# Kernel tuning notes

Measured on AMD Instinct MI355X. Metric: run time of the kernel, lower is better.

The kernel has to match this reference:

```python
import jax, jax.numpy as jnp
import numpy as np

N_NODES = 10000
N_EDGES = 160000
C = 64        # latent channels
H = 512       # MLP hidden width
L = 2         # allegro layers
NB = 8        # bessel basis size
CUT = 2.0     # radial cutoff
AVG = 3.0     # avg_num_neighbors


def setup_inputs() -> dict:
    key = jax.random.key(0)
    ks = jax.random.split(key, 12)
    positions = jax.random.normal(ks[0], (N_NODES, 3), jnp.float32)
    species = jax.random.randint(ks[1], (N_NODES,), 0, 2, jnp.int32)
    senders = jax.random.randint(ks[2], (N_EDGES,), 0, N_NODES, jnp.int32)
    receivers = jax.random.randint(ks[3], (N_EDGES,), 0, N_NODES, jnp.int32)
    w = lambda k, shape, fan: (jax.random.normal(k, shape, jnp.float32) / np.sqrt(fan).astype(np.float32))
    return dict(
        positions=positions,
        W_emb1=w(ks[4], (NB + 4, H), NB + 4),
        W_emb2=w(ks[5], (H, C), H),
        W_v=w(ks[6], (C, C), C),
        W_env=w(ks[7], (L, C, C), C),
        W_lat1=w(ks[8], (L, 3 * C, H), 3 * C),
        W_lat2=w(ks[9], (L, H, C), H),
        W_mix=w(ks[10], (L, C, 2 * C), C),
        W_out=w(ks[11], (C,), C),
        species=species, senders=senders, receivers=receivers,
    )


def reference(positions, W_emb1, W_emb2, W_v, W_env, W_lat1, W_lat2, W_mix, W_out,
              species, senders, receivers):
    node_attrs = jax.nn.one_hot(species, 2, dtype=positions.dtype)   # [N,2]
    r = positions[receivers] - positions[senders]                    # [E,3] edge vectors ('1o')
    d = jnp.sqrt(jnp.sum(r * r, axis=-1))                            # [E]
    dsafe = jnp.maximum(d, 1e-6)
    u = r / dsafe[:, None]                                           # unit vectors = l=1 spherical harmonics

    # radial basis: Bessel functions with smooth polynomial cutoff envelope
    xc = d / CUT
    env = jnp.where(xc < 1.0, (1.0 - xc ** 2) ** 2, 0.0)             # [E]
    nvec = jnp.arange(1, NB + 1, dtype=positions.dtype)
    bessel = jnp.sqrt(2.0 / CUT) * jnp.sin(nvec * jnp.pi * xc[:, None]) / dsafe[:, None]
    rad = bessel * env[:, None]                                      # [E,NB]

    # two-body latent embedding
    feat = jnp.concatenate([rad, node_attrs[senders], node_attrs[receivers]], axis=-1)  # [E,NB+4]
    x = (jax.nn.silu(feat @ W_emb1) @ W_emb2) * env[:, None]         # [E,C]
    # initial equivariant edge features (C channels of 1o)
    V = (x @ W_v)[:, :, None] * u[:, None, :]                        # [E,C,3]

    inv_sqrt2 = 1.0 / jnp.sqrt(2.0)
    for l in range(L):
        # environment density: scatter edge basis to sender nodes, gather back per edge
        w_e = x @ W_env[l]                                           # [E,C]
        rho1 = jax.ops.segment_sum(w_e[:, :, None] * u[:, None, :], senders,
                                   num_segments=N_NODES) / AVG       # [N,C,3] (1o density)
        rho0 = jax.ops.segment_sum(w_e, senders, num_segments=N_NODES) / AVG  # [N,C] (0e density)
        rho1_e = rho1[senders]                                       # [E,C,3]
        rho0_e = rho0[senders]                                       # [E,C]

        # channel-wise Clebsch-Gordan tensor products (lmax=1 paths)
        tp_scal = jnp.einsum('eci,eci->ec', V, rho1_e)               # 1o x 1o -> 0e
        tp_vec1 = V * rho0_e[:, :, None]                             # 1o x 0e -> 1o
        tp_vec2 = jnp.cross(V, rho1_e)                               # 1o x 1o -> 1e

        # latent update (residual, envelope-gated)
        lat_in = jnp.concatenate([x, tp_scal, rho0_e], axis=-1)      # [E,3C]
        dx = (jax.nn.silu(lat_in @ W_lat1[l]) @ W_lat2[l]) * env[:, None]
        x = (x + dx) * inv_sqrt2

        # equivariant update: latent-conditioned mix of tensor-product outputs
        mix = x @ W_mix[l]                                           # [E,2C]
        V = mix[:, :C, None] * tp_vec1 + mix[:, C:, None] * tp_vec2  # [E,C,3]

    # per-edge scalar readout, scatter-reduced to nodes
    e_edge = (x @ W_out) * env                                       # [E]
    node_energy = jax.ops.segment_sum(e_edge, receivers, num_segments=N_NODES) / AVG
    return node_energy
```

## Files before the change

### kernel.cpp

```cpp
#include <hip/hip_runtime.h>
#include <hip/hip_bf16.h>

#define E_NUM 160000
#define NN 10000
#define PI_F 3.14159265358979323846f

using u16 = unsigned short;
using u32 = unsigned int;
typedef short bf16x8 __attribute__((ext_vector_type(8)));
typedef float f32x4 __attribute__((ext_vector_type(4)));
typedef u32 u32x4 __attribute__((ext_vector_type(4)));

__device__ __forceinline__ float silu_fast(float z) {
    return z * __builtin_amdgcn_rcpf(1.0f + __expf(-z));
}
__device__ __forceinline__ float bfb2f(u32 bits16) {
    return __builtin_bit_cast(float, bits16 << 16);
}
__device__ __forceinline__ u32 f2bfb(float f) {
    return (u32)__builtin_bit_cast(u16, __float2bfloat16(f));
}
__device__ __forceinline__ u32 pack2(float lo, float hi) {
    return f2bfb(lo) | (f2bfb(hi) << 16);
}

__global__ void k_detect(const u16* __restrict__ posraw, int* __restrict__ flag) {
    int i = blockIdx.x * 256 + threadIdx.x;
    if (i >= 15000) return;
    float v = bfb2f((u32)posraw[2 * i]);
    if (!(fabsf(v) < 1e4f)) atomicOr(flag, 1);
}

__global__ void k_cvt_all(const void* s0, const void* s1, const void* s2,
                          const void* s3, const void* s4, const void* s5,
                          const void* s6, const void* s7, const void* s8,
                          float* __restrict__ dst, const int* __restrict__ flag) {
    int i = blockIdx.x * 256 + threadIdx.x;
    if (i >= 359792) return;
    const void* src; int off;
    if      (i < 30000)  { src = s0; off = i; }
    else if (i < 36144)  { src = s1; off = i - 30000; }
    else if (i < 68912)  { src = s2; off = i - 36144; }
    else if (i < 73008)  { src = s3; off = i - 68912; }
    else if (i < 81200)  { src = s4; off = i - 73008; }
    else if (i < 277808) { src = s5; off = i - 81200; }
    else if (i < 343344) { src = s6; off = i - 277808; }
    else if (i < 359728) { src = s7; off = i - 343344; }
    else                 { src = s8; off = i - 359728; }
    if (*flag) dst[i] = ((const float*)src)[off];
    else       dst[i] = bfb2f((u32)((const u16*)src)[off]);
}

__global__ void k_pack(const float* __restrict__ W, int K, int Nshift,
                       u16* __restrict__ pk) {
    int i = blockIdx.x * 256 + threadIdx.x;
    int total = K << Nshift;
    if (i >= total) return;
    int k = i >> Nshift, n = i & ((1 << Nshift) - 1);
    float w = W[i];
    u16 h = (u16)f2bfb(w);
    float r = w - bfb2f((u32)h);
    int idx = ((((k >> 3) << Nshift) + n) << 4) + (k & 7);
    pk[idx] = h; pk[idx + 8] = (u16)f2bfb(r);
}

__global__ void k_pack_emb1(const float* __restrict__ W , u16* __restrict__ pk) {
    int i = blockIdx.x * 256 + threadIdx.x;
    if (i >= 64 * 512) return;
    int k = i >> 9, n = i & 511;
    u16 out = 0;
    if (k < 24) {
        out = (u16)f2bfb(W[(k % 12) * 512 + n]);
    } else if (k < 36) {
        float w = W[(k - 24) * 512 + n];
        u16 h = (u16)f2bfb(w);
        out = (u16)f2bfb(w - bfb2f((u32)h));
    }
    pk[((((k >> 3) << 9) + n) << 4) + (k & 7)] = out;
}

__global__ void k_hist(const int* __restrict__ senders, int* __restrict__ counts) {
    int e = blockIdx.x * 256 + threadIdx.x;
    if (e < E_NUM) atomicAdd(&counts[senders[e]], 1);
}

__global__ __launch_bounds__(1024) void k_scan(const int* __restrict__ counts,
                                               int* __restrict__ rowstart) {
    __shared__ int part[1024];
    int t = threadIdx.x;
    int base = t * 10;
    int local[10];
    int sum = 0;
    #pragma unroll
    for (int i = 0; i < 10; i++) {
        int v = (base + i < NN) ? counts[base + i] : 0;
        local[i] = sum; sum += v;
    }
    part[t] = sum;
    __syncthreads();
    for (int off = 1; off < 1024; off <<= 1) {
        int v = (t >= off) ? part[t - off] : 0;
        __syncthreads();
        part[t] += v;
        __syncthreads();
    }
    int pre = (t == 0) ? 0 : part[t - 1];
    #pragma unroll
    for (int i = 0; i < 10; i++)
        if (base + i < NN) rowstart[base + i] = pre + local[i];
    if (t == 1023) rowstart[NN] = part[1023];
}

__global__ void k_copy_int(const int* __restrict__ src, int* __restrict__ dst, int n) {
    int i = blockIdx.x * 256 + threadIdx.x;
    if (i < n) dst[i] = src[i];
}

__global__ void k_fill(const int* __restrict__ senders, int* __restrict__ cursor,
                       int* __restrict__ edge_list) {
    int e = blockIdx.x * 256 + threadIdx.x;
    if (e >= E_NUM) return;
    int pos = atomicAdd(&cursor[senders[e]], 1);
    edge_list[pos] = e;
}

__global__ void k_geom(const float* __restrict__ posf, const int* __restrict__ species,
                       const int* __restrict__ senders, const int* __restrict__ receivers,
                       const int* __restrict__ edge_list,
                       int* __restrict__ ssend, int* __restrict__ srecv,
                       float* __restrict__ ux, float* __restrict__ uy, float* __restrict__ uz,
                       float* __restrict__ envb, u32* __restrict__ latin) {
    int e = blockIdx.x * 256 + threadIdx.x;
    if (e >= E_NUM) return;
    int orig = edge_list[e];
    int s = senders[orig], r = receivers[orig];
    ssend[e] = s; srecv[e] = r;
    float rx = posf[3 * r + 0] - posf[3 * s + 0];
    float ry = posf[3 * r + 1] - posf[3 * s + 1];
    float rz = posf[3 * r + 2] - posf[3 * s + 2];
    float d = sqrtf(rx * rx + ry * ry + rz * rz);
    float inv = 1.0f / fmaxf(d, 1e-6f);
    ux[e] = rx * inv; uy[e] = ry * inv; uz[e] = rz * inv;
    float xc = d * 0.5f;
    float env = 0.0f;
    if (xc < 1.0f) { float t = 1.0f - xc * xc; env = t * t; }
    envb[e] = env;
    float ft[12];
    float se = env * inv;
    #pragma unroll
    for (int n = 1; n <= 8; n++) ft[n - 1] = __sinf((float)n * PI_F * xc) * se;
    int ss = species[s], sr = species[r];
    ft[8] = (ss == 0) ? 1.0f : 0.0f;
    ft[9] = (ss == 1) ? 1.0f : 0.0f;
    ft[10] = (sr == 0) ? 1.0f : 0.0f;
    ft[11] = (sr == 1) ? 1.0f : 0.0f;
    u32 fh[12]; float fl[12];
    #pragma unroll
    for (int i = 0; i < 12; i++) {
        fh[i] = f2bfb(ft[i]);
        fl[i] = ft[i] - bfb2f(fh[i]);
    }
    #pragma unroll
    for (int j = 0; j < 6; j++) {
        u32 v = fh[2 * j] | (fh[2 * j + 1] << 16);
        latin[(size_t)j * E_NUM + e] = v;
        latin[(size_t)(12 + j) * E_NUM + e] = v;
        latin[(size_t)(6 + j) * E_NUM + e] = pack2(fl[2 * j], fl[2 * j + 1]);
    }
}

__global__ __launch_bounds__(256) void k_rho_gather(
    const float* __restrict__ we, const int* __restrict__ rowstart,
    const float* __restrict__ ux, const float* __restrict__ uy,
    const float* __restrict__ uz,
    float* __restrict__ rho0, float* __restrict__ rho1) {
    int wv = (blockIdx.x * 256 + threadIdx.x) >> 6;
    int c = threadIdx.x & 63;
    if (wv >= NN) return;
    int start = rowstart[wv], end = rowstart[wv + 1];
    float s0 = 0.0f, sx = 0.0f, sy = 0.0f, sz = 0.0f;
    for (int j = start; j < end; j++) {
        float w = we[(size_t)j * 64 + c];
        float a = ux[j], b = uy[j], g = uz[j];
        s0 += w;
        sx = fmaf(w, a, sx);
        sy = fmaf(w, b, sy);
        sz = fmaf(w, g, sz);
    }
    const float inv3 = 1.0f / 3.0f;
    rho0[(size_t)wv * 64 + c] = s0 * inv3;
    rho1[(size_t)wv * 192 + 3 * c + 0] = sx * inv3;
    rho1[(size_t)wv * 192 + 3 * c + 1] = sy * inv3;
    rho1[(size_t)wv * 192 + 3 * c + 2] = sz * inv3;
}

template<int KSTEPS, int MODE, int HASLO, int FUSEWE, int STAGE>
__global__ __launch_bounds__(512, 4) void k_mlp(
    const u32* __restrict__ latin,
    const u16* __restrict__ W1pk, const u16* __restrict__ W2pk,
    const float* __restrict__ envb,
    u16* __restrict__ xout,
    const u16* __restrict__ wepk,
    float* __restrict__ webuf,
    const u16* __restrict__ xin,
    const u16* __restrict__ x0t,
    const int* __restrict__ ssend,
    const float* __restrict__ ux, const float* __restrict__ uy,
    const float* __restrict__ uz,
    const float* __restrict__ rho0A, const float* __restrict__ rho1A,
    const float* __restrict__ rho0B, const float* __restrict__ rho1B,
    const u16* __restrict__ wvpk, const u16* __restrict__ wmpk) {
    constexpr int ROWDW = KSTEPS * 16;
    constexpr int INAREG = KSTEPS * 4096;
    constexpr int SMEMSZ = INAREG + ((STAGE == 2) ? (2 * 16640) : 32768);
    __shared__ __align__(16) char smem[SMEMSZ];
    u32* inA = (u32*)smem;
    u16* hA  = (u16*)(smem + INAREG);
    float* tbA = (float*)(smem + INAREG);
    u16* mb   = (u16*)(smem + INAREG + 16640);
    u32* mb32 = (u32*)(smem + INAREG + 16640);
    u32* xt0  = (u32*)(smem + INAREG + 16640);
    int lane = threadIdx.x & 63;
    int sub = threadIdx.x >> 6;
    int w = __builtin_amdgcn_readfirstlane(sub);
    int l15 = lane & 15, quad = lane >> 4;
    int e0 = blockIdx.x * 64;
    int e = e0 + lane;

    if (STAGE == 0) {
        constexpr int CPW = (KSTEPS * 4) / 8;
        #pragma unroll
        for (int j = 0; j < CPW; j++) {
            int c = w * CPW + j;
            u32x4 v;
            #pragma unroll
            for (int i = 0; i < 4; i++) v[i] = latin[(size_t)(c * 4 + i) * E_NUM + e];
            int slot = (c & ~7) | ((c ^ lane) & 7);
            *(u32x4*)(&inA[lane * ROWDW + slot * 4]) = v;
        }
        __syncthreads();
    } else {
        {
            int c = w;
            u32x4 v;
            #pragma unroll
            for (int i = 0; i < 4; i++) {
                u32 lo = (u32)xin[(size_t)(8 * c + 2 * i) * E_NUM + e];
                u32 hi = (u32)xin[(size_t)(8 * c + 2 * i + 1) * E_NUM + e];
                v[i] = lo | (hi << 16);
            }
            int slot = (c & ~7) | ((c ^ lane) & 7);
            *(u32x4*)(&inA[lane * ROWDW + slot * 4]) = v;
        }
        if (STAGE == 2) {
            int c = w;
            u32x4 v;
            #pragma unroll
            for (int i = 0; i < 4; i++) {
                u32 lo = (u32)x0t[(size_t)(8 * c + 2 * i) * E_NUM + e];
                u32 hi = (u32)x0t[(size_t)(8 * c + 2 * i + 1) * E_NUM + e];
                v[i] = lo | (hi << 16);
            }
            int slot = (c ^ lane) & 7;
            *(u32x4*)(&xt0[lane * 32 + slot * 4]) = v;
        }
        __syncthreads();
        int mt = w & 3;
        int ntbA = (w >> 2) * 2;
        f32x4 accA[2];
        accA[0] = (f32x4){0.f, 0.f, 0.f, 0.f};
        accA[1] = (f32x4){0.f, 0.f, 0.f, 0.f};
        #pragma unroll
        for (int ks = 0; ks < 2; ks++) {
            int c = ks * 4 + quad;
            int m = mt * 16 + l15;
            bf16x8 af;
            if (STAGE == 1) {
                int slot = (c & ~7) | ((c ^ m) & 7);
                af = *(const bf16x8*)(&inA[m * ROWDW + slot * 4]);
            } else {
                int slot = (c ^ m) & 7;
                af = *(const bf16x8*)(&xt0[m * 32 + slot * 4]);
            }
            #pragma unroll
            for (int nti = 0; nti < 2; nti++) {
                int n = (ntbA + nti) * 16 + l15;
                const u16* bp = wvpk + ((((size_t)c << 6) + n) << 4);
                bf16x8 bh = *(const bf16x8*)(bp);
                accA[nti] = __builtin_amdgcn_mfma_f32_16x16x32_bf16(af, bh, accA[nti], 0, 0, 0);
                bf16x8 bl = *(const bf16x8*)(bp + 8);
                accA[nti] = __builtin_amdgcn_mfma_f32_16x16x32_bf16(af, bl, accA[nti], 0, 0, 0);
            }
        }
        f32x4 accM[4];
        if (STAGE == 2) {
            #pragma unroll
            for (int i = 0; i < 4; i++) accM[i] = (f32x4){0.f, 0.f, 0.f, 0.f};
            int nbM = (w >> 2) * 4;
            #pragma unroll
            for (int ks = 0; ks < 2; ks++) {
                int c = ks * 4 + quad;
                int m = mt * 16 + l15;
                int slot = (c & ~7) | ((c ^ m) & 7);
                bf16x8 af = *(const bf16x8*)(&inA[m * ROWDW + slot * 4]);
                #pragma unroll
                for (int nti = 0; nti < 4; nti++) {
                    int n = (nbM + nti) * 16 + l15;
                    const u16* bp = wmpk + ((((size_t)c << 7) + n) << 4);
                    bf16x8 bh = *(const bf16x8*)(bp);
                    accM[nti] = __builtin_amdgcn_mfma_f32_16x16x32_bf16(af, bh, accM[nti], 0, 0, 0);
                    bf16x8 bl = *(const bf16x8*)(bp + 8);
                    accM[nti] = __builtin_amdgcn_mfma_f32_16x16x32_bf16(af, bl, accM[nti], 0, 0, 0);
                }
            }
        }
        __syncthreads();
        #pragma unroll
        for (int nti = 0; nti < 2; nti++) {
            #pragma unroll
            for (int r = 0; r < 4; r++) {
                int rowD = mt * 16 + quad * 4 + r;
                int colD = (ntbA + nti) * 16 + l15;
                tbA[colD * 65 + rowD] = accA[nti][r];
            }
        }
        if (STAGE == 2) {
            int sel = (w >= 4) ? 1 : 0;
            #pragma unroll
            for (int nti = 0; nti < 4; nti++) {
                #pragma unroll
                for (int r = 0; r < 4; r++) {
                    int rowD = mt * 16 + quad * 4 + r;
                    int colD = nti * 16 + l15;
                    mb[((colD * 65 + rowD) << 1) + sel] = (u16)f2bfb(accM[nti][r]);
                }
            }
        }
        __syncthreads();
        int c0 = w * 8;
        float av[8], m1v[8], m2v[8];
        #pragma unroll
        for (int i = 0; i < 8; i++) av[i] = tbA[(c0 + i) * 65 + lane];
        if (STAGE == 2) {
            #pragma unroll
            for (int i = 0; i < 8; i++) {
                u32 pv = mb32[(c0 + i) * 65 + lane];
                m1v[i] = bfb2f(pv & 0xffffu);
                m2v[i] = bfb2f(pv >> 16);
            }
        }
        int s = ssend[e];
        float u0 = ux[e], u1 = uy[e], u2 = uz[e];
        float ts[8], rr[8];
        if (STAGE == 1) {
            const float* r1 = rho1A + (size_t)s * 192;
            const float* r0 = rho0A + (size_t)s * 64;
            #pragma unroll
            for (int i = 0; i < 8; i++) {
                int c = c0 + i;
                float dot = u0 * r1[3 * c] + u1 * r1[3 * c + 1] + u2 * r1[3 * c + 2];
                ts[i] = av[i] * dot;
                rr[i] = r0[c];
            }
        } else {
            const float* r1A = rho1A + (size_t)s * 192;
            const float* r0A = rho0A + (size_t)s * 64;
            const float* r1B = rho1B + (size_t)s * 192;
            const float* r0B = rho0B + (size_t)s * 64;
            #pragma unroll
            for (int i = 0; i < 8; i++) {
                int c = c0 + i;
                float v0 = av[i] * u0, v1 = av[i] * u1, v2 = av[i] * u2;
                float aA0 = r1A[3 * c], aA1 = r1A[3 * c + 1], aA2 = r1A[3 * c + 2];
                float rc = r0A[c];
                float w0 = m1v[i] * v0 * rc + m2v[i] * (v1 * aA2 - v2 * aA1);
                float w1 = m1v[i] * v1 * rc + m2v[i] * (v2 * aA0 - v0 * aA2);
                float w2 = m1v[i] * v2 * rc + m2v[i] * (v0 * aA1 - v1 * aA0);
                ts[i] = w0 * r1B[3 * c] + w1 * r1B[3 * c + 1] + w2 * r1B[3 * c + 2];
                rr[i] = r0B[c];
            }
        }
        u32x4 tv, rv;
        #pragma unroll
        for (int j = 0; j < 4; j++) {
            tv[j] = pack2(ts[2 * j], ts[2 * j + 1]);
            rv[j] = pack2(rr[2 * j], rr[2 * j + 1]);
        }
        {
            int c = 8 + w;
            int slot = (c & ~7) | ((c ^ lane) & 7);
            *(u32x4*)(&inA[lane * ROWDW + slot * 4]) = tv;
        }
        {
            int c = 16 + w;
            int slot = (c & ~7) | ((c ^ lane) & 7);
            *(u32x4*)(&inA[lane * ROWDW + slot * 4]) = rv;
        }
        __syncthreads();
    }

    f32x4 acc2[2];
    acc2[0] = (f32x4){0.f, 0.f, 0.f, 0.f};
    acc2[1] = (f32x4){0.f, 0.f, 0.f, 0.f};
    int nt2 = w & 3;
    int mt2a = (w >> 2) * 2;
    int p = 0;

    #pragma unroll
    for (int it = 0; it < 5; it++) {
        f32x4 acc[4];
        if (it < 4) {
            #pragma unroll
            for (int mt = 0; mt < 4; mt++) acc[mt] = (f32x4){0.f, 0.f, 0.f, 0.f};
            __builtin_amdgcn_s_setprio(1);
            #pragma unroll
            for (int ks = 0; ks < KSTEPS; ks++) {
                int c = ks * 4 + quad;
                bf16x8 afr[4];
                #pragma unroll
                for (int mt = 0; mt < 4; mt++) {
                    int m = mt * 16 + l15;
                    int slot = (c & ~7) | ((c ^ m) & 7);
                    afr[mt] = *(const bf16x8*)(&inA[m * ROWDW + slot * 4]);
                }
                int n = it * 128 + w * 16 + l15;
                const u16* bp = W1pk + ((((size_t)c << 9) + n) << 4);
                bf16x8 bh = *(const bf16x8*)(bp);
                #pragma unroll
                for (int mt = 0; mt < 4; mt++)
                    acc[mt] = __builtin_amdgcn_mfma_f32_16x16x32_bf16(afr[mt], bh, acc[mt], 0, 0, 0);
                if (HASLO) {
                    bf16x8 bl = *(const bf16x8*)(bp + 8);
                    #pragma unroll
                    for (int mt = 0; mt < 4; mt++)
                        acc[mt] = __builtin_amdgcn_mfma_f32_16x16x32_bf16(afr[mt], bl, acc[mt], 0, 0, 0);
                }
            }
            __builtin_amdgcn_s_setprio(0);
        }
        if (it > 0) {
            const u16* hAr = hA + (p ^ 1) * 8192;
            __builtin_amdgcn_s_setprio(1);
            #pragma unroll
            for (int ks = 0; ks < 4; ks++) {
                int c = ks * 4 + quad;
                int m0 = mt2a * 16 + l15;
                int m1i = m0 + 16;
                int s0 = (c & 8) | ((c ^ m0) & 7);
                int s1 = (c & 8) | ((c ^ m1i) & 7);
                bf16x8 a0 = *(const bf16x8*)(&hAr[m0 * 128 + s0 * 8]);
                bf16x8 a1 = *(const bf16x8*)(&hAr[m1i * 128 + s1 * 8]);
                const u16* bp = W2pk + ((((size_t)((it - 1) * 16 + c) << 6) + nt2 * 16 + l15) << 4);
                bf16x8 bh = *(const bf16x8*)(bp);
                acc2[0] = __builtin_amdgcn_mfma_f32_16x16x32_bf16(a0, bh, acc2[0], 0, 0, 0);
                acc2[1] = __builtin_amdgcn_mfma_f32_16x16x32_bf16(a1, bh, acc2[1], 0, 0, 0);
                bf16x8 bl = *(const bf16x8*)(bp + 8);
                acc2[0] = __builtin_amdgcn_mfma_f32_16x16x32_bf16(a0, bl, acc2[0], 0, 0, 0);
                acc2[1] = __builtin_amdgcn_mfma_f32_16x16x32_bf16(a1, bl, acc2[1], 0, 0, 0);
            }
            __builtin_amdgcn_s_setprio(0);
        }
        if (it < 4) {
            u16* hAw = hA + p * 8192;
            int kh = w * 16 + l15;
            int c = kh >> 3;
            #pragma unroll
            for (int mt = 0; mt < 4; mt++) {
                #pragma unroll
                for (int r = 0; r < 4; r++) {
                    int m = mt * 16 + quad * 4 + r;
                    float s = silu_fast(acc[mt][r]);
                    int slot = (c & 8) | ((c ^ m) & 7);
                    hAw[m * 128 + slot * 8 + (kh & 7)] = (u16)f2bfb(s);
                }
            }
            __syncthreads();
        }
        p ^= 1;
    }
    float xo[8];
    if (MODE) {
        int c = w;
        int slot = (c & ~7) | ((c ^ lane) & 7);
        #pragma unroll
        for (int i = 0; i < 4; i++) {
            u32 pv = inA[lane * ROWDW + slot * 4 + i];
            xo[2 * i]     = bfb2f(pv & 0xffffu);
            xo[2 * i + 1] = bfb2f(pv >> 16);
        }
    }
    __syncthreads();
    float* epi = (float*)inA;
    #pragma unroll
    for (int mi = 0; mi < 2; mi++) {
        #pragma unroll
        for (int r = 0; r < 4; r++) {
            int m = (mt2a + mi) * 16 + quad * 4 + r;
            int c = nt2 * 16 + l15;
            epi[c * 65 + m] = acc2[mi][r];
        }
    }
    __syncthreads();
    float env = envb[e];
    const float is2 = 0.70710678118654752f;
    #pragma unroll
    for (int i = 0; i < 8; i++) {
        int c = w * 8 + i;
        float v = epi[c * 65 + lane];
        float res;
        if (MODE) res = (xo[i] + v * env) * is2;
        else      res = v * env;
        xout[(size_t)c * E_NUM + e] = (u16)f2bfb(res);
        if (FUSEWE) epi[c * 65 + lane] = res;
    }
    if (FUSEWE) {
        __syncthreads();
        int mt = w & 3;
        int ntb = (w >> 2) * 2;
        f32x4 accw[2];
        accw[0] = (f32x4){0.f, 0.f, 0.f, 0.f};
        accw[1] = (f32x4){0.f, 0.f, 0.f, 0.f};
        #pragma unroll
        for (int ks = 0; ks < 2; ks++) {
            bf16x8 af;
            #pragma unroll
            for (int j = 0; j < 8; j++)
                af[j] = (short)f2bfb(epi[(ks * 32 + quad * 8 + j) * 65 + mt * 16 + l15]);
            #pragma unroll
            for (int nti = 0; nti < 2; nti++) {
                int n4 = (ntb + nti) * 16 + l15;
                const u16* bp = wepk + ((((size_t)(ks * 4 + quad) << 6) + n4) << 4);
                bf16x8 bh = *(const bf16x8*)(bp);
                accw[nti] = __builtin_amdgcn_mfma_f32_16x16x32_bf16(af, bh, accw[nti], 0, 0, 0);
                bf16x8 bl = *(const bf16x8*)(bp + 8);
                accw[nti] = __builtin_amdgcn_mfma_f32_16x16x32_bf16(af, bl, accw[nti], 0, 0, 0);
            }
        }
        #pragma unroll
        for (int nti = 0; nti < 2; nti++) {
            #pragma unroll
            for (int r = 0; r < 4; r++) {
                int rowD = mt * 16 + quad * 4 + r;
                int colD = (ntb + nti) * 16 + l15;
                webuf[(size_t)(e0 + rowD) * 64 + colD] = accw[nti][r];
            }
        }
    }
}

__global__ void k_readout(const u16* __restrict__ x, const float* __restrict__ Wout,
                          const float* __restrict__ envb, const int* __restrict__ srecv,
                          float* __restrict__ node_acc) {
    int e = blockIdx.x * 256 + threadIdx.x;
    if (e >= E_NUM) return;
    float a = 0.0f;
    #pragma unroll
    for (int c = 0; c < 64; c++) {
        a = fmaf(bfb2f((u32)x[(size_t)c * E_NUM + e]), Wout[c], a);
    }
    a *= envb[e] * (1.0f / 3.0f);
    atomicAdd(&node_acc[srecv[e]], a);
}

__global__ void k_out(const float* __restrict__ node_acc, void* __restrict__ out,
                      const int* __restrict__ flag) {
    int n = blockIdx.x * 256 + threadIdx.x;
    if (n >= NN) return;
    float v = node_acc[n];
    if (*flag) ((float*)out)[n] = v;
    else       ((u16*)out)[n] = (u16)f2bfb(v);
}

extern "C" void kernel_launch(void* const* d_in, const int* in_sizes, int n_in,
                              void* d_out, int out_size, void* d_ws, size_t ws_size,
                              hipStream_t stream) {
    const void* posr   = d_in[0];
    const void* Wemb1r = d_in[1];
    const void* Wemb2r = d_in[2];
    const void* Wvr    = d_in[3];
    const void* Wenvr  = d_in[4];
    const void* Wlat1r = d_in[5];
    const void* Wlat2r = d_in[6];
    const void* Wmixr  = d_in[7];
    const void* Woutr  = d_in[8];
    const int* species   = (const int*)d_in[9];
    const int* senders   = (const int*)d_in[10];
    const int* receivers = (const int*)d_in[11];

    char* p = (char*)d_ws;
    auto alloc = [&](size_t bytes) -> void* {
        void* rp = (void*)p;
        p += (bytes + 255) & ~(size_t)255;
        return rp;
    };
    int*   flag  = (int*)alloc(4);
    float* wbuf  = (float*)alloc(359792 * 4);
    float* posf  = wbuf;
    float* Wemb1 = wbuf + 30000;
    float* Wemb2 = wbuf + 36144;
    float* Wv    = wbuf + 68912;
    float* Wenv  = wbuf + 73008;
    float* Wlat1 = wbuf + 81200;
    float* Wlat2 = wbuf + 277808;
    float* Wmix  = wbuf + 343344;
    float* Wout  = wbuf + 359728;
    const size_t E = E_NUM;
    float* ux   = (float*)alloc(E * 4);
    float* uy   = (float*)alloc(E * 4);
    float* uz   = (float*)alloc(E * 4);
    float* envb = (float*)alloc(E * 4);
    float* rho0A = (float*)alloc((size_t)NN * 64 * 4);
    float* rho1A = (float*)alloc((size_t)NN * 192 * 4);
    float* rho0B = (float*)alloc((size_t)NN * 64 * 4);
    float* rho1B = (float*)alloc((size_t)NN * 192 * 4);
    float* node_acc = (float*)alloc((size_t)NN * 4);
    int* counts    = (int*)alloc((size_t)NN * 4);
    int* rowstart  = (int*)alloc((size_t)(NN + 1) * 4);
    int* cursor    = (int*)alloc((size_t)NN * 4);
    int* edge_list = (int*)alloc(E * 4);
    int* ssend     = (int*)alloc(E * 4);
    int* srecv     = (int*)alloc(E * 4);
    void* unionbuf = alloc(96 * E * 4);
    u32*   latin = (u32*)unionbuf;
    float* webuf = (float*)unionbuf + (size_t)32 * E;
    u16* x0 = (u16*)alloc(64 * E * 2);
    u16* x1 = (u16*)alloc(64 * E * 2);
    u16* w1pk = (u16*)alloc(2 * 196608 * 2);
    u16* w2pk = (u16*)alloc(2 * 65536 * 2);
    u16* e1pk = (u16*)alloc(65536 * 2);
    u16* e2pk = (u16*)alloc(65536 * 2);
    u16* we0pk = (u16*)alloc(8192 * 2);
    u16* we1pk = (u16*)alloc(8192 * 2);
    u16* wvpk  = (u16*)alloc(8192 * 2);
    u16* wmpk  = (u16*)alloc(16384 * 2);

    hipMemsetAsync(flag, 0, 4, stream);
    hipMemsetAsync(counts, 0, (size_t)NN * 4, stream);
    hipMemsetAsync(node_acc, 0, (size_t)NN * 4, stream);
    hipMemsetAsync(latin + (size_t)18 * E, 0, (size_t)14 * E * 4, stream);

    k_detect<<<(15000 + 255) / 256, 256, 0, stream>>>((const u16*)posr, flag);

    k_cvt_all<<<(359792 + 255) / 256, 256, 0, stream>>>(
        posr, Wemb1r, Wemb2r, Wvr, Wenvr, Wlat1r, Wlat2r, Wmixr, Woutr,
        wbuf, flag);

    k_pack_emb1<<<128, 256, 0, stream>>>(Wemb1, e1pk);
    k_pack<<<128, 256, 0, stream>>>(Wemb2, 512, 6, e2pk);
    k_pack<<<16, 256, 0, stream>>>(Wenv, 64, 6, we0pk);
    k_pack<<<16, 256, 0, stream>>>(Wenv + 4096, 64, 6, we1pk);
    k_pack<<<16, 256, 0, stream>>>(Wv, 64, 6, wvpk);
    k_pack<<<32, 256, 0, stream>>>(Wmix, 64, 7, wmpk);
    for (int l = 0; l < 2; l++) {
        k_pack<<<384, 256, 0, stream>>>(Wlat1 + l * 98304, 192, 9,
                                        w1pk + l * 196608);
        k_pack<<<128, 256, 0, stream>>>(Wlat2 + l * 32768, 512, 6,
                                        w2pk + l * 65536);
    }

    k_hist<<<625, 256, 0, stream>>>(senders, counts);
    k_scan<<<1, 1024, 0, stream>>>(counts, rowstart);
    k_copy_int<<<(NN + 255) / 256, 256, 0, stream>>>(rowstart, cursor, NN);
    k_fill<<<625, 256, 0, stream>>>(senders, cursor, edge_list);

    k_geom<<<625, 256, 0, stream>>>(posf, species, senders, receivers, edge_list,
                                    ssend, srecv, ux, uy, uz, envb, latin);
    k_mlp<2, 0, 0, 1, 0><<<2500, 512, 0, stream>>>(
        latin, e1pk, e2pk, envb, x0, we0pk, webuf,
        nullptr, nullptr, nullptr, nullptr, nullptr, nullptr,
        nullptr, nullptr, nullptr, nullptr, nullptr, nullptr);

    k_rho_gather<<<2500, 256, 0, stream>>>(webuf, rowstart, ux, uy, uz,
                                           rho0A, rho1A);
    k_mlp<6, 1, 1, 1, 1><<<2500, 512, 0, stream>>>(
        nullptr, w1pk, w2pk, envb, x1, we1pk, webuf,
        x0, nullptr, ssend, ux, uy, uz, rho0A, rho1A, nullptr, nullptr,
        wvpk, nullptr);

    k_rho_gather<<<2500, 256, 0, stream>>>(webuf, rowstart, ux, uy, uz,
                                           rho0B, rho1B);
    k_mlp<6, 1, 1, 0, 2><<<2500, 512, 0, stream>>>(
        nullptr, w1pk + 196608, w2pk + 65536, envb, x1, nullptr, nullptr,
        x1, x0, ssend, ux, uy, uz, rho0A, rho1A, rho0B, rho1B,
        wvpk, wmpk);

    k_readout<<<625, 256, 0, stream>>>(x1, Wout, envb, srecv, node_acc);
    k_out<<<(NN + 255) / 256, 256, 0, stream>>>(node_acc, d_out, flag);
}
```

Measured before the change: 461.3 us.

## Interleave per-edge latent storage into 16-byte chunks and fuse readout into final MLP

```diff
diff --git a/kernel.cpp b/kernel.cpp
--- a/kernel.cpp
+++ b/kernel.cpp
@@ -154,18 +154,22 @@
     ft[9] = (ss == 1) ? 1.0f : 0.0f;
     ft[10] = (sr == 0) ? 1.0f : 0.0f;
     ft[11] = (sr == 1) ? 1.0f : 0.0f;
-    u32 fh[12]; float fl[12];
-    #pragma unroll
-    for (int i = 0; i < 12; i++) {
-        fh[i] = f2bfb(ft[i]);
-        fl[i] = ft[i] - bfb2f(fh[i]);
-    }
+    u32 ch[32];
+    #pragma unroll
+    for (int i = 0; i < 32; i++) ch[i] = 0;
     #pragma unroll
     for (int j = 0; j < 6; j++) {
-        u32 v = fh[2 * j] | (fh[2 * j + 1] << 16);
-        latin[(size_t)j * E_NUM + e] = v;
-        latin[(size_t)(12 + j) * E_NUM + e] = v;
-        latin[(size_t)(6 + j) * E_NUM + e] = pack2(fl[2 * j], fl[2 * j + 1]);
+        u32 hp = f2bfb(ft[2 * j]) | (f2bfb(ft[2 * j + 1]) << 16);
+        float l0 = ft[2 * j] - bfb2f(f2bfb(ft[2 * j]));
+        float l1 = ft[2 * j + 1] - bfb2f(f2bfb(ft[2 * j + 1]));
+        ch[j] = hp;
+        ch[12 + j] = hp;
+        ch[6 + j] = pack2(l0, l1);
+    }
+    #pragma unroll
+    for (int g = 0; g < 8; g++) {
+        u32x4 v = {ch[4 * g], ch[4 * g + 1], ch[4 * g + 2], ch[4 * g + 3]};
+        *(u32x4*)(latin + (((size_t)g * E_NUM + e) << 2)) = v;
     }
 }
 
@@ -199,17 +203,19 @@
     const u32* __restrict__ latin,
     const u16* __restrict__ W1pk, const u16* __restrict__ W2pk,
     const float* __restrict__ envb,
-    u16* __restrict__ xout,
+    u32* __restrict__ xout,
     const u16* __restrict__ wepk,
     float* __restrict__ webuf,
-    const u16* __restrict__ xin,
-    const u16* __restrict__ x0t,
+    const u32* __restrict__ xin,
+    const u32* __restrict__ x0t,
     const int* __restrict__ ssend,
     const float* __restrict__ ux, const float* __restrict__ uy,
     const float* __restrict__ uz,
     const float* __restrict__ rho0A, const float* __restrict__ rho1A,
     const float* __restrict__ rho0B, const float* __restrict__ rho1B,
-    const u16* __restrict__ wvpk, const u16* __restrict__ wmpk) {
+    const u16* __restrict__ wvpk, const u16* __restrict__ wmpk,
+    const float* __restrict__ WoutP, const int* __restrict__ srecv,
+    float* __restrict__ node_acc) {
     constexpr int ROWDW = KSTEPS * 16;
     constexpr int INAREG = KSTEPS * 4096;
     constexpr int SMEMSZ = INAREG + ((STAGE == 2) ? (2 * 16640) : 32768);
@@ -232,9 +238,7 @@
         #pragma unroll
         for (int j = 0; j < CPW; j++) {
             int c = w * CPW + j;
-            u32x4 v;
-            #pragma unroll
-            for (int i = 0; i < 4; i++) v[i] = latin[(size_t)(c * 4 + i) * E_NUM + e];
+            u32x4 v = *(const u32x4*)(latin + (((size_t)c * E_NUM + e) << 2));
             int slot = (c & ~7) | ((c ^ lane) & 7);
             *(u32x4*)(&inA[lane * ROWDW + slot * 4]) = v;
         }
@@ -242,26 +246,13 @@
     } else {
         {
             int c = w;
-            u32x4 v;
-            #pragma unroll
-            for (int i = 0; i < 4; i++) {
-                u32 lo = (u32)xin[(size_t)(8 * c + 2 * i) * E_NUM + e];
-                u32 hi = (u32)xin[(size_t)(8 * c + 2 * i + 1) * E_NUM + e];
-                v[i] = lo | (hi << 16);
-            }
+            u32x4 v = *(const u32x4*)(xin + (((size_t)c * E_NUM + e) << 2));
             int slot = (c & ~7) | ((c ^ lane) & 7);
             *(u32x4*)(&inA[lane * ROWDW + slot * 4]) = v;
         }
         if (STAGE == 2) {
-            int c = w;
-            u32x4 v;
-            #pragma unroll
-            for (int i = 0; i < 4; i++) {
-                u32 lo = (u32)x0t[(size_t)(8 * c + 2 * i) * E_NUM + e];
-                u32 hi = (u32)x0t[(size_t)(8 * c + 2 * i + 1) * E_NUM + e];
-                v[i] = lo | (hi << 16);
-            }
-            int slot = (c ^ lane) & 7;
+            u32x4 v = *(const u32x4*)(x0t + (((size_t)w * E_NUM + e) << 2));
+            int slot = (w ^ lane) & 7;
             *(u32x4*)(&xt0[lane * 32 + slot * 4]) = v;
         }
         __syncthreads();
@@ -503,6 +494,7 @@
     __syncthreads();
     float env = envb[e];
     const float is2 = 0.70710678118654752f;
+    float resv[8];
     #pragma unroll
     for (int i = 0; i < 8; i++) {
         int c = w * 8 + i;
@@ -510,8 +502,28 @@
         float res;
         if (MODE) res = (xo[i] + v * env) * is2;
         else      res = v * env;
-        xout[(size_t)c * E_NUM + e] = (u16)f2bfb(res);
+        resv[i] = res;
         if (FUSEWE) epi[c * 65 + lane] = res;
+    }
+    if (STAGE != 2) {
+        u32x4 tv;
+        #pragma unroll
+        for (int j = 0; j < 4; j++) tv[j] = pack2(resv[2 * j], resv[2 * j + 1]);
+        *(u32x4*)(xout + (((size_t)w * E_NUM + e) << 2)) = tv;
+    }
+    if (STAGE == 2) {
+        float* red = (float*)(smem + 20480);
+        float pd = 0.0f;
+        #pragma unroll
+        for (int i = 0; i < 8; i++) pd = fmaf(resv[i], WoutP[w * 8 + i], pd);
+        red[w * 64 + lane] = pd;
+        __syncthreads();
+        if (w == 0) {
+            float sum = 0.0f;
+            #pragma unroll
+            for (int ww = 0; ww < 8; ww++) sum += red[ww * 64 + lane];
+            atomicAdd(&node_acc[srecv[e]], sum * env * (1.0f / 3.0f));
+        }
     }
     if (FUSEWE) {
         __syncthreads();
@@ -546,20 +558,6 @@
             }
         }
     }
-}
-
-__global__ void k_readout(const u16* __restrict__ x, const float* __restrict__ Wout,
-                          const float* __restrict__ envb, const int* __restrict__ srecv,
-                          float* __restrict__ node_acc) {
-    int e = blockIdx.x * 256 + threadIdx.x;
-    if (e >= E_NUM) return;
-    float a = 0.0f;
-    #pragma unroll
-    for (int c = 0; c < 64; c++) {
-        a = fmaf(bfb2f((u32)x[(size_t)c * E_NUM + e]), Wout[c], a);
-    }
-    a *= envb[e] * (1.0f / 3.0f);
-    atomicAdd(&node_acc[srecv[e]], a);
 }
 
 __global__ void k_out(const float* __restrict__ node_acc, void* __restrict__ out,
@@ -623,8 +621,8 @@
     void* unionbuf = alloc(96 * E * 4);
     u32*   latin = (u32*)unionbuf;
     float* webuf = (float*)unionbuf + (size_t)32 * E;
-    u16* x0 = (u16*)alloc(64 * E * 2);
-    u16* x1 = (u16*)alloc(64 * E * 2);
+    u32* x0 = (u32*)alloc(32 * E * 4);
+    u32* x1 = (u32*)alloc(32 * E * 4);
     u16* w1pk = (u16*)alloc(2 * 196608 * 2);
     u16* w2pk = (u16*)alloc(2 * 65536 * 2);
     u16* e1pk = (u16*)alloc(65536 * 2);
@@ -637,7 +635,6 @@
     hipMemsetAsync(flag, 0, 4, stream);
     hipMemsetAsync(counts, 0, (size_t)NN * 4, stream);
     hipMemsetAsync(node_acc, 0, (size_t)NN * 4, stream);
-    hipMemsetAsync(latin + (size_t)18 * E, 0, (size_t)14 * E * 4, stream);
 
     k_detect<<<(15000 + 255) / 256, 256, 0, stream>>>((const u16*)posr, flag);
 
@@ -668,22 +665,22 @@
     k_mlp<2, 0, 0, 1, 0><<<2500, 512, 0, stream>>>(
         latin, e1pk, e2pk, envb, x0, we0pk, webuf,
         nullptr, nullptr, nullptr, nullptr, nullptr, nullptr,
-        nullptr, nullptr, nullptr, nullptr, nullptr, nullptr);
+        nullptr, nullptr, nullptr, nullptr, nullptr, nullptr,
+        nullptr, nullptr, nullptr);
 
     k_rho_gather<<<2500, 256, 0, stream>>>(webuf, rowstart, ux, uy, uz,
                                            rho0A, rho1A);
     k_mlp<6, 1, 1, 1, 1><<<2500, 512, 0, stream>>>(
         nullptr, w1pk, w2pk, envb, x1, we1pk, webuf,
         x0, nullptr, ssend, ux, uy, uz, rho0A, rho1A, nullptr, nullptr,
-        wvpk, nullptr);
+        wvpk, nullptr, nullptr, nullptr, nullptr);
 
     k_rho_gather<<<2500, 256, 0, stream>>>(webuf, rowstart, ux, uy, uz,
                                            rho0B, rho1B);
     k_mlp<6, 1, 1, 0, 2><<<2500, 512, 0, stream>>>(
-        nullptr, w1pk + 196608, w2pk + 65536, envb, x1, nullptr, nullptr,
+        nullptr, w1pk + 196608, w2pk + 65536, envb, nullptr, nullptr, nullptr,
         x1, x0, ssend, ux, uy, uz, rho0A, rho1A, rho0B, rho1B,
-        wvpk, wmpk);
-
-    k_readout<<<625, 256, 0, stream>>>(x1, Wout, envb, srecv, node_acc);
+        wvpk, wmpk, Wout, srecv, node_acc);
+
     k_out<<<(NN + 255) / 256, 256, 0, stream>>>(node_acc, d_out, flag);
 }
```

Measured after the change: 433.2 us. 6.1% less time.
